# Kernel tuning notes

Measured on AMD Instinct MI355X. Metric: run time of the kernel, lower is better.

The kernel has to match this reference:

```python
import jax, jax.numpy as jnp
import numpy as np

COS_EPS = 1e-8  # torch F.cosine_similarity eps


def setup_inputs() -> dict:
    key = jax.random.key(0)
    k1, k2 = jax.random.split(key)
    x = jax.random.normal(k1, (8192, 512), dtype=jnp.float32)
    class_logits = jax.random.normal(k2, (8192, 100), dtype=jnp.float32)
    return {"x": x, "class_logits": class_logits}


def reference(x, class_logits):
    N, D = x.shape
    C = class_logits.shape[1]

    # class_logits.clone().detach()
    logits = jax.lax.stop_gradient(class_logits)
    pred = jax.nn.softmax(logits, axis=1)
    max_logit = pred.max(axis=1)          # [N]
    max_cls = pred.argmax(axis=1)         # [N] int

    # graph(): pairwise cosine similarity = normalize rows + gram matmul
    norms = jnp.linalg.norm(x, axis=1, keepdims=True)
    xn = x / jnp.maximum(norms, COS_EPS)
    mat = xn @ xn.T                       # [N, N]

    x_agg = mat @ x + x                   # [N, D]
    x_new = jax.lax.stop_gradient(x_agg)

    # update_prototype: per-class weighted scatter-add then mean over counts
    weighted = x_new * max_logit[:, None]                     # [N, D]
    sums = jax.ops.segment_sum(weighted, max_cls, num_segments=C)      # [C, D]
    counts = jax.ops.segment_sum(jnp.ones((N,), x.dtype), max_cls, num_segments=C)  # [C]
    prototypes = jnp.where(counts[:, None] > 0,
                           sums / jnp.maximum(counts, 1.0)[:, None],
                           jnp.zeros_like(sums))              # [C, D]

    # inter_class_matrix[i, j] = prototypes[j] - prototypes[i]
    inter_class_matrix = prototypes[None, :, :] - prototypes[:, None, :]  # [C, C, D]
    return prototypes, inter_class_matrix
```

## Files before the change

kernel.cpp:

```cpp
#include <hip/hip_runtime.h>
#include <math.h>

#define N_ROWS 8192
#define D_DIM  512
#define C_CLS  100

typedef unsigned short u16;
typedef unsigned int u32;
typedef __attribute__((ext_vector_type(8))) short short8;
typedef __attribute__((ext_vector_type(4))) float floatx4;

#define WS_G      0
#define WS_GP     262144
#define WS_INV    5505024
#define WS_SINV   5513216
#define WS_WV     5521408
#define WS_CLS    5529600
#define WS_CNT    5537792
#define WS_OFFS   5537920
#define WS_ORDER  5538048
#define WS_ZTH    5546240
#define WS_ZTL    7643392
#define WS_U      9740544
#define WS_V      9791744

__device__ __forceinline__ void split2(float v, u16& h, u16& l) {
    unsigned u = __float_as_uint(v);
    h = (u16)(u >> 16);
    float r = v - __uint_as_float(u & 0xFFFF0000u);
    l = (u16)(__float_as_uint(r) >> 16);
}

typedef const __attribute__((address_space(1))) u32* gp32;
typedef __attribute__((address_space(3))) u32* lp32;
__device__ __forceinline__ void cp16(const u16* g, u16* l) {
    __builtin_amdgcn_global_load_lds((gp32)g, (lp32)l, 16, 0, 0);
}

__global__ __launch_bounds__(256) void k_prep(const float* __restrict__ logits,
        const float* __restrict__ x, float* __restrict__ wv,
        int* __restrict__ cls, float* __restrict__ inv, float* __restrict__ sinv) {
    int wave = (blockIdx.x * blockDim.x + threadIdx.x) >> 6;
    int lane = threadIdx.x & 63;
    if (wave >= N_ROWS) return;
    const float* row = logits + (size_t)wave * C_CLS;
    float v1 = row[lane];
    bool has2 = (lane + 64) < C_CLS;
    float v2 = has2 ? row[lane + 64] : -INFINITY;
    float m; int idx;
    if (v2 > v1) { m = v2; idx = lane + 64; } else { m = v1; idx = lane; }
    #pragma unroll
    for (int off = 32; off >= 1; off >>= 1) {
        float om = __shfl_down(m, off);
        int   oi = __shfl_down(idx, off);
        if (om > m || (om == m && oi < idx)) { m = om; idx = oi; }
    }
    m = __shfl(m, 0);
    idx = __shfl(idx, 0);
    float s = expf(v1 - m) + (has2 ? expf(v2 - m) : 0.0f);
    #pragma unroll
    for (int off = 32; off >= 1; off >>= 1) s += __shfl_down(s, off);
    const float* xr = x + (size_t)wave * D_DIM;
    float ss = 0.f;
    #pragma unroll
    for (int j = 0; j < D_DIM; j += 64) {
        float v = xr[j + lane];
        ss += v * v;
    }
    #pragma unroll
    for (int off = 32; off >= 1; off >>= 1) ss += __shfl_down(ss, off);
    if (lane == 0) {
        wv[wave] = 1.0f / s;
        cls[wave] = idx;
        float iv = 1.0f / fmaxf(sqrtf(ss), 1e-8f);
        inv[wave] = iv;
        sinv[wave] = sqrtf(iv);
    }
}

#define LDT 65
__global__ __launch_bounds__(256) void k_mid(const float* __restrict__ x,
        const float* __restrict__ sinv, const int* __restrict__ cls,
        u16* __restrict__ zth, u16* __restrict__ ztl,
        int* __restrict__ cnt, int* __restrict__ offs, int* __restrict__ order) {
    __shared__ unsigned zt_p[64 * LDT];
    int bx = blockIdx.x;
    int t = threadIdx.x;
    if (bx == 1024) {
        __shared__ int hist[128], scan_s[128], cur[128];
        if (t < 128) hist[t] = 0;
        __syncthreads();
        for (int m2 = t; m2 < N_ROWS; m2 += 256) atomicAdd(&hist[cls[m2]], 1);
        __syncthreads();
        if (t < 128) scan_s[t] = hist[t];
        __syncthreads();
        #pragma unroll
        for (int d = 1; d < 128; d <<= 1) {
            int add = 0;
            if (t < 128 && t >= d) add = scan_s[t - d];
            __syncthreads();
            if (t < 128) scan_s[t] += add;
            __syncthreads();
        }
        if (t < 128) {
            int off0 = scan_s[t] - hist[t];
            cur[t] = off0;
            offs[t] = off0;
            cnt[t] = hist[t];
        }
        __syncthreads();
        for (int m2 = t; m2 < N_ROWS; m2 += 256) {
            int c2 = cls[m2];
            int p = atomicAdd(&cur[c2], 1);
            order[p] = m2;
        }
        return;
    }
    int r0 = (bx & 127) << 6, c0 = (bx >> 7) << 6;
    int r = t >> 2, cq = t & 3;
    const float* src = x + (size_t)(r0 + r) * D_DIM + c0 + cq * 16;
    float vv[16];
    {
        float4 a = *(const float4*)(src + 0);
        float4 b = *(const float4*)(src + 4);
        float4 c = *(const float4*)(src + 8);
        float4 d = *(const float4*)(src + 12);
        vv[0]=a.x; vv[1]=a.y; vv[2]=a.z; vv[3]=a.w;
        vv[4]=b.x; vv[5]=b.y; vv[6]=b.z; vv[7]=b.w;
        vv[8]=c.x; vv[9]=c.y; vv[10]=c.z; vv[11]=c.w;
        vv[12]=d.x; vv[13]=d.y; vv[14]=d.z; vv[15]=d.w;
    }
    float sv = sinv[r0 + r];
    #pragma unroll
    for (int j = 0; j < 16; ++j) {
        u16 h, l;
        split2(sv * vv[j], h, l);
        zt_p[(cq * 16 + j) * LDT + r] = ((unsigned)h << 16) | l;
    }
    __syncthreads();
    int c = t >> 2, rq = (t & 3) * 16;
    size_t tbase = (size_t)(c0 + c) * N_ROWS + r0 + rq;
    uint oh[8], ol[8];
    #pragma unroll
    for (int p = 0; p < 8; ++p) {
        unsigned d0 = zt_p[c * LDT + rq + 2*p];
        unsigned d1 = zt_p[c * LDT + rq + 2*p + 1];
        oh[p] = (d0 >> 16) | (d1 & 0xFFFF0000u);
        ol[p] = (d0 & 0xFFFFu) | (d1 << 16);
    }
    *(uint4*)&zth[tbase]     = make_uint4(oh[0], oh[1], oh[2], oh[3]);
    *(uint4*)&zth[tbase + 8] = make_uint4(oh[4], oh[5], oh[6], oh[7]);
    *(uint4*)&ztl[tbase]     = make_uint4(ol[0], ol[1], ol[2], ol[3]);
    *(uint4*)&ztl[tbase + 8] = make_uint4(ol[4], ol[5], ol[6], ol[7]);
}

__global__ __launch_bounds__(256) void k_big(const u16* __restrict__ zth,
        const u16* __restrict__ ztl, const float* __restrict__ x,
        const float* __restrict__ inv, const float* __restrict__ wv,
        const int* __restrict__ order, const int* __restrict__ offs,
        const int* __restrict__ cnt, float* __restrict__ Gp,
        float* __restrict__ u, float* __restrict__ v) {
    __shared__ __attribute__((aligned(16))) u16 Ah[128*32], Al[128*32];
    __shared__ __attribute__((aligned(16))) u16 Bh[128*32], Bl[128*32];
    __shared__ float us[4][64], vs[4][64];
    int bx = blockIdx.x;
    int t = threadIdx.x;
    if (bx >= 320) {
        int idx = bx - 320;
        int c = idx >> 3, jc = idx & 7;
        int g = t >> 6, lane = t & 63;
        int j = jc * 64 + lane;
        int n = cnt[c], o = offs[c];
        float ua = 0.f, va = 0.f;
        for (int p = g; p < n; p += 4) {
            int m = order[o + p];
            float wm = wv[m];
            float wi = wm * inv[m];
            float xv = x[(size_t)m * D_DIM + j];
            ua += wi * xv; va += wm * xv;
        }
        us[g][lane] = ua; vs[g][lane] = va;
        __syncthreads();
        if (g == 0) {
            u[(size_t)c * D_DIM + j] = us[0][lane] + us[1][lane] + us[2][lane] + us[3][lane];
            v[(size_t)c * D_DIM + j] = vs[0][lane] + vs[1][lane] + vs[2][lane] + vs[3][lane];
        }
        return;
    }
    int tile = bx % 10;
    int p = bx / 10;
    int ti = tile < 4 ? 0 : (tile < 7 ? 1 : (tile < 9 ? 2 : 3));
    int tj = tile - (ti == 0 ? 0 : (ti == 1 ? 3 : (ti == 2 ? 5 : 6)));
    int i0 = ti << 7, j0 = tj << 7;
    bool diag = (ti == tj);
    int kb = p << 8;
    int w = t >> 6, l = t & 63;
    int srow = t >> 2, scol = (t & 3) << 3;
    int lm = l & 15, lg = l >> 4;
    floatx4 acc[4][4];
    #pragma unroll
    for (int mi = 0; mi < 4; ++mi)
        #pragma unroll
        for (int ni = 0; ni < 4; ++ni) acc[mi][ni] = (floatx4){0.f,0.f,0.f,0.f};
    int d0 = srow * 32 + scol;
    int d1 = (64 + srow) * 32 + scol;
    const size_t ga0 = (size_t)(i0 + srow) * N_ROWS + kb + scol;
    const size_t ga1 = (size_t)(i0 + 64 + srow) * N_ROWS + kb + scol;
    const size_t gb0 = (size_t)(j0 + srow) * N_ROWS + kb + scol;
    const size_t gb1 = (size_t)(j0 + 64 + srow) * N_ROWS + kb + scol;
    const u16* Bhs = diag ? Ah : Bh;
    const u16* Bls = diag ? Al : Bl;
    for (int s = 0; s < 8; ++s) {
        int ks = s << 5;
        cp16(zth + ga0 + ks, Ah + d0);
        cp16(zth + ga1 + ks, Ah + d1);
        cp16(ztl + ga0 + ks, Al + d0);
        cp16(ztl + ga1 + ks, Al + d1);
        if (!diag) {
            cp16(zth + gb0 + ks, Bh + d0);
            cp16(zth + gb1 + ks, Bh + d1);
            cp16(ztl + gb0 + ks, Bl + d0);
            cp16(ztl + gb1 + ks, Bl + d1);
        }
        __syncthreads();
        short8 ah[4], al[4], bh[4], bl[4];
        #pragma unroll
        for (int mi = 0; mi < 4; ++mi) {
            int off = (((w & 1) << 6) + (mi << 4) + lm) * 32 + (lg << 3);
            ah[mi] = *(const short8*)&Ah[off];
            al[mi] = *(const short8*)&Al[off];
        }
        #pragma unroll
        for (int ni = 0; ni < 4; ++ni) {
            int off = (((w >> 1) << 6) + (ni << 4) + lm) * 32 + (lg << 3);
            bh[ni] = *(const short8*)&Bhs[off];
            bl[ni] = *(const short8*)&Bls[off];
        }
        #pragma unroll
        for (int mi = 0; mi < 4; ++mi)
            #pragma unroll
            for (int ni = 0; ni < 4; ++ni) {
                acc[mi][ni] = __builtin_amdgcn_mfma_f32_16x16x32_bf16(ah[mi], bh[ni], acc[mi][ni], 0, 0, 0);
                acc[mi][ni] = __builtin_amdgcn_mfma_f32_16x16x32_bf16(ah[mi], bl[ni], acc[mi][ni], 0, 0, 0);
                acc[mi][ni] = __builtin_amdgcn_mfma_f32_16x16x32_bf16(al[mi], bh[ni], acc[mi][ni], 0, 0, 0);
            }
        __syncthreads();
    }
    float* Gb = Gp + ((size_t)(p * 10 + tile) << 14);
    #pragma unroll
    for (int mi = 0; mi < 4; ++mi) {
        int row0 = ((w & 1) << 6) + (mi << 4) + (lg << 2);
        #pragma unroll
        for (int ni = 0; ni < 4; ++ni) {
            int col = ((w >> 1) << 6) + (ni << 4) + lm;
            #pragma unroll
            for (int r = 0; r < 4; ++r)
                Gb[(size_t)(row0 + r) * 128 + col] = acc[mi][ni][r];
        }
    }
}

__global__ void k_reduceG(const float* __restrict__ Gp, float* __restrict__ G) {
    int i = blockIdx.x * 256 + threadIdx.x;
    int r = i >> 9, c = i & 511;
    int tr = r >> 7, tc = c >> 7, rr = r & 127, cc = c & 127;
    if (tr > tc) { int tmp = tr; tr = tc; tc = tmp; tmp = rr; rr = cc; cc = tmp; }
    int tid = tr * 4 + tc - ((tr * (tr + 1)) >> 1);
    const float* src = Gp + ((size_t)tid << 14) + rr * 128 + cc;
    float s = 0.f;
    #pragma unroll
    for (int p = 0; p < 32; ++p) s += src[(size_t)p * 163840];
    G[i] = s;
}

__global__ __launch_bounds__(256) void k_pgemm(const float* __restrict__ u,
        const float* __restrict__ v, const int* __restrict__ cnt,
        const float* __restrict__ G, float* __restrict__ out) {
    __shared__ float us[D_DIM];
    int c = blockIdx.x >> 1;
    int j = ((blockIdx.x & 1) << 8) + threadIdx.x;
    us[threadIdx.x]       = u[(size_t)c * D_DIM + threadIdx.x];
    us[threadIdx.x + 256] = u[(size_t)c * D_DIM + threadIdx.x + 256];
    __syncthreads();
    float acc = v[(size_t)c * D_DIM + j];
    #pragma unroll 8
    for (int k = 0; k < D_DIM; ++k)
        acc += us[k] * G[(size_t)k * D_DIM + j];
    int n = cnt[c];
    float s = (n > 0) ? 1.0f / (float)n : 0.0f;
    out[(size_t)c * D_DIM + j] = acc * s;
}

__global__ void k_inter(const float* __restrict__ proto, float* __restrict__ out) {
    int pair = blockIdx.x;
    int i = pair / C_CLS;
    int j = pair - i * C_CLS;
    int d = threadIdx.x << 2;
    float4 pj = *(const float4*)&proto[j * D_DIM + d];
    float4 pi = *(const float4*)&proto[i * D_DIM + d];
    float4 r;
    r.x = pj.x - pi.x; r.y = pj.y - pi.y; r.z = pj.z - pi.z; r.w = pj.w - pi.w;
    *(float4*)&out[(size_t)pair * D_DIM + d] = r;
}

extern "C" void kernel_launch(void* const* d_in, const int* in_sizes, int n_in,
                              void* d_out, int out_size, void* d_ws, size_t ws_size,
                              hipStream_t stream) {
    const float* x      = (const float*)d_in[0];
    const float* logits = (const float*)d_in[1];
    float* out = (float*)d_out;
    float* ws  = (float*)d_ws;
    float* G     = ws + WS_G;
    float* Gp    = ws + WS_GP;
    float* inv   = ws + WS_INV;
    float* sinv  = ws + WS_SINV;
    float* wv    = ws + WS_WV;
    int*   cls   = (int*)(ws + WS_CLS);
    int*   cnt   = (int*)(ws + WS_CNT);
    int*   offs  = (int*)(ws + WS_OFFS);
    int*   order = (int*)(ws + WS_ORDER);
    u16* zth = (u16*)(ws + WS_ZTH);
    u16* ztl = (u16*)(ws + WS_ZTL);
    float* u_arr = ws + WS_U;
    float* v_arr = ws + WS_V;

    k_prep<<<N_ROWS / 4, 256, 0, stream>>>(logits, x, wv, cls, inv, sinv);
    k_mid<<<1025, 256, 0, stream>>>(x, sinv, cls, zth, ztl, cnt, offs, order);
    k_big<<<1120, 256, 0, stream>>>(zth, ztl, x, inv, wv, order, offs, cnt, Gp, u_arr, v_arr);
    k_reduceG<<<D_DIM * D_DIM / 256, 256, 0, stream>>>(Gp, G);
    k_pgemm<<<C_CLS * 2, 256, 0, stream>>>(u_arr, v_arr, cnt, G, out);
    k_inter<<<C_CLS * C_CLS, 128, 0, stream>>>(out, out + C_CLS * D_DIM);
}
```

Before: 178.8 us.

## Fuse prep kernels, replace split-K partial buffer with atomic accumulation

Folds row-norm computation, softmax stats and the hi/lo transpose split into one kernel, and moves the class histogram into its own single-block kernel. The Gram kernel now runs with a split-K depth of 512 instead of 256, halving the grid, and accumulates its tiles straight into G with float atomics, mirroring off-diagonal tiles, so the partial buffer and reduction kernel go away. The inter-class difference kernel handles 4 pairs per block with 8 floats per thread. This cuts launches and the partial-buffer traffic, at the cost of heavy atomic contention (16 partitions per element, doubled for off-diagonal tiles), nondeterministic summation order, and less parallelism in the GEMM.

```diff
diff --git a/kernel.cpp b/kernel.cpp
--- a/kernel.cpp
+++ b/kernel.cpp
@@ -11,18 +11,18 @@
 typedef __attribute__((ext_vector_type(4))) float floatx4;
 
 #define WS_G      0
-#define WS_GP     262144
-#define WS_INV    5505024
-#define WS_SINV   5513216
-#define WS_WV     5521408
-#define WS_CLS    5529600
-#define WS_CNT    5537792
-#define WS_OFFS   5537920
-#define WS_ORDER  5538048
-#define WS_ZTH    5546240
-#define WS_ZTL    7643392
-#define WS_U      9740544
-#define WS_V      9791744
+#define WS_INV    262144
+#define WS_WV     270336
+#define WS_CLS    278528
+#define WS_CNT    286720
+#define WS_OFFS   286848
+#define WS_ORDER  286976
+#define WS_U      295168
+#define WS_V      346368
+#define WS_ZTH    397568
+#define WS_ZTL    2494720
+
+#define LDT 65
 
 __device__ __forceinline__ void split2(float v, u16& h, u16& l) {
     unsigned u = __float_as_uint(v);
@@ -37,136 +37,151 @@
     __builtin_amdgcn_global_load_lds((gp32)g, (lp32)l, 16, 0, 0);
 }
 
-__global__ __launch_bounds__(256) void k_prep(const float* __restrict__ logits,
-        const float* __restrict__ x, float* __restrict__ wv,
-        int* __restrict__ cls, float* __restrict__ inv, float* __restrict__ sinv) {
-    int wave = (blockIdx.x * blockDim.x + threadIdx.x) >> 6;
-    int lane = threadIdx.x & 63;
-    if (wave >= N_ROWS) return;
-    const float* row = logits + (size_t)wave * C_CLS;
-    float v1 = row[lane];
-    bool has2 = (lane + 64) < C_CLS;
-    float v2 = has2 ? row[lane + 64] : -INFINITY;
-    float m; int idx;
-    if (v2 > v1) { m = v2; idx = lane + 64; } else { m = v1; idx = lane; }
+__global__ __launch_bounds__(256) void kA(const float* __restrict__ logits,
+        const float* __restrict__ x, float* __restrict__ wv, int* __restrict__ cls,
+        float* __restrict__ inv, u16* __restrict__ zth, u16* __restrict__ ztl,
+        float* __restrict__ G) {
+    __shared__ unsigned zt_p[64 * LDT];
+    __shared__ float ns[4][64];
+    __shared__ float sv_s[64];
+    int bx = blockIdx.x, t = threadIdx.x;
+    if (bx < 2048) {
+        int row = (bx << 2) + (t >> 6);
+        int lane = t & 63;
+        const float* lrow = logits + (size_t)row * C_CLS;
+        float v1 = lrow[lane];
+        bool has2 = (lane + 64) < C_CLS;
+        float v2 = has2 ? lrow[lane + 64] : -INFINITY;
+        float m; int idx;
+        if (v2 > v1) { m = v2; idx = lane + 64; } else { m = v1; idx = lane; }
+        #pragma unroll
+        for (int off = 32; off >= 1; off >>= 1) {
+            float om = __shfl_down(m, off);
+            int   oi = __shfl_down(idx, off);
+            if (om > m || (om == m && oi < idx)) { m = om; idx = oi; }
+        }
+        m = __shfl(m, 0);
+        idx = __shfl(idx, 0);
+        float s = expf(v1 - m) + (has2 ? expf(v2 - m) : 0.0f);
+        #pragma unroll
+        for (int off = 32; off >= 1; off >>= 1) s += __shfl_down(s, off);
+        if (lane == 0) {
+            wv[row] = 1.0f / s;
+            cls[row] = idx;
+        }
+        return;
+    }
+    if (bx >= 2176) {
+        int i = ((bx - 2176) * 256 + t) * 32;
+        float4 z = make_float4(0.f, 0.f, 0.f, 0.f);
+        #pragma unroll
+        for (int q = 0; q < 8; ++q) *(float4*)&G[i + q * 4] = z;
+        return;
+    }
+    int r0 = (bx - 2048) << 6;
+    {
+        int l = t & 63, q = t >> 6;
+        const float* src = x + (size_t)(r0 + l) * D_DIM + q * 128;
+        float ss = 0.f;
+        #pragma unroll
+        for (int i = 0; i < 32; ++i) {
+            float4 v = *(const float4*)(src + i * 4);
+            ss += v.x * v.x + v.y * v.y + v.z * v.z + v.w * v.w;
+        }
+        ns[q][l] = ss;
+    }
+    __syncthreads();
+    if (t < 64) {
+        float ss = ns[0][t] + ns[1][t] + ns[2][t] + ns[3][t];
+        float iv = 1.0f / fmaxf(sqrtf(ss), 1e-8f);
+        inv[r0 + t] = iv;
+        sv_s[t] = sqrtf(iv);
+    }
+    __syncthreads();
+    for (int ct = 0; ct < 8; ++ct) {
+        int c0 = ct * 64;
+        int r = t >> 2, cq = t & 3;
+        const float* src = x + (size_t)(r0 + r) * D_DIM + c0 + cq * 16;
+        float vv[16];
+        {
+            float4 a = *(const float4*)(src + 0);
+            float4 b = *(const float4*)(src + 4);
+            float4 c = *(const float4*)(src + 8);
+            float4 d = *(const float4*)(src + 12);
+            vv[0]=a.x; vv[1]=a.y; vv[2]=a.z; vv[3]=a.w;
+            vv[4]=b.x; vv[5]=b.y; vv[6]=b.z; vv[7]=b.w;
+            vv[8]=c.x; vv[9]=c.y; vv[10]=c.z; vv[11]=c.w;
+            vv[12]=d.x; vv[13]=d.y; vv[14]=d.z; vv[15]=d.w;
+        }
+        float sv = sv_s[r];
+        #pragma unroll
+        for (int j = 0; j < 16; ++j) {
+            u16 h, l;
+            split2(sv * vv[j], h, l);
+            zt_p[(cq * 16 + j) * LDT + r] = ((unsigned)h << 16) | l;
+        }
+        __syncthreads();
+        int c = t >> 2, rq = (t & 3) * 16;
+        size_t tbase = (size_t)(c0 + c) * N_ROWS + r0 + rq;
+        uint oh[8], ol[8];
+        #pragma unroll
+        for (int p = 0; p < 8; ++p) {
+            unsigned d0 = zt_p[c * LDT + rq + 2*p];
+            unsigned d1 = zt_p[c * LDT + rq + 2*p + 1];
+            oh[p] = (d0 >> 16) | (d1 & 0xFFFF0000u);
+            ol[p] = (d0 & 0xFFFFu) | (d1 << 16);
+        }
+        *(uint4*)&zth[tbase]     = make_uint4(oh[0], oh[1], oh[2], oh[3]);
+        *(uint4*)&zth[tbase + 8] = make_uint4(oh[4], oh[5], oh[6], oh[7]);
+        *(uint4*)&ztl[tbase]     = make_uint4(ol[0], ol[1], ol[2], ol[3]);
+        *(uint4*)&ztl[tbase + 8] = make_uint4(ol[4], ol[5], ol[6], ol[7]);
+        __syncthreads();
+    }
+}
+
+__global__ __launch_bounds__(256) void kB(const int* __restrict__ cls,
+        int* __restrict__ cnt, int* __restrict__ offs, int* __restrict__ order) {
+    __shared__ int hist[128], scan_s[128], cur[128];
+    int t = threadIdx.x;
+    if (t < 128) hist[t] = 0;
+    __syncthreads();
+    for (int m = t; m < N_ROWS; m += 256) atomicAdd(&hist[cls[m]], 1);
+    __syncthreads();
+    if (t < 128) scan_s[t] = hist[t];
+    __syncthreads();
     #pragma unroll
-    for (int off = 32; off >= 1; off >>= 1) {
-        float om = __shfl_down(m, off);
-        int   oi = __shfl_down(idx, off);
-        if (om > m || (om == m && oi < idx)) { m = om; idx = oi; }
-    }
-    m = __shfl(m, 0);
-    idx = __shfl(idx, 0);
-    float s = expf(v1 - m) + (has2 ? expf(v2 - m) : 0.0f);
-    #pragma unroll
-    for (int off = 32; off >= 1; off >>= 1) s += __shfl_down(s, off);
-    const float* xr = x + (size_t)wave * D_DIM;
-    float ss = 0.f;
-    #pragma unroll
-    for (int j = 0; j < D_DIM; j += 64) {
-        float v = xr[j + lane];
-        ss += v * v;
-    }
-    #pragma unroll
-    for (int off = 32; off >= 1; off >>= 1) ss += __shfl_down(ss, off);
-    if (lane == 0) {
-        wv[wave] = 1.0f / s;
-        cls[wave] = idx;
-        float iv = 1.0f / fmaxf(sqrtf(ss), 1e-8f);
-        inv[wave] = iv;
-        sinv[wave] = sqrtf(iv);
-    }
-}
-
-#define LDT 65
-__global__ __launch_bounds__(256) void k_mid(const float* __restrict__ x,
-        const float* __restrict__ sinv, const int* __restrict__ cls,
-        u16* __restrict__ zth, u16* __restrict__ ztl,
-        int* __restrict__ cnt, int* __restrict__ offs, int* __restrict__ order) {
-    __shared__ unsigned zt_p[64 * LDT];
-    int bx = blockIdx.x;
-    int t = threadIdx.x;
-    if (bx == 1024) {
-        __shared__ int hist[128], scan_s[128], cur[128];
-        if (t < 128) hist[t] = 0;
-        __syncthreads();
-        for (int m2 = t; m2 < N_ROWS; m2 += 256) atomicAdd(&hist[cls[m2]], 1);
-        __syncthreads();
-        if (t < 128) scan_s[t] = hist[t];
-        __syncthreads();
-        #pragma unroll
-        for (int d = 1; d < 128; d <<= 1) {
-            int add = 0;
-            if (t < 128 && t >= d) add = scan_s[t - d];
-            __syncthreads();
-            if (t < 128) scan_s[t] += add;
-            __syncthreads();
-        }
-        if (t < 128) {
-            int off0 = scan_s[t] - hist[t];
-            cur[t] = off0;
-            offs[t] = off0;
-            cnt[t] = hist[t];
-        }
-        __syncthreads();
-        for (int m2 = t; m2 < N_ROWS; m2 += 256) {
-            int c2 = cls[m2];
-            int p = atomicAdd(&cur[c2], 1);
-            order[p] = m2;
-        }
-        return;
-    }
-    int r0 = (bx & 127) << 6, c0 = (bx >> 7) << 6;
-    int r = t >> 2, cq = t & 3;
-    const float* src = x + (size_t)(r0 + r) * D_DIM + c0 + cq * 16;
-    float vv[16];
-    {
-        float4 a = *(const float4*)(src + 0);
-        float4 b = *(const float4*)(src + 4);
-        float4 c = *(const float4*)(src + 8);
-        float4 d = *(const float4*)(src + 12);
-        vv[0]=a.x; vv[1]=a.y; vv[2]=a.z; vv[3]=a.w;
-        vv[4]=b.x; vv[5]=b.y; vv[6]=b.z; vv[7]=b.w;
-        vv[8]=c.x; vv[9]=c.y; vv[10]=c.z; vv[11]=c.w;
-        vv[12]=d.x; vv[13]=d.y; vv[14]=d.z; vv[15]=d.w;
-    }
-    float sv = sinv[r0 + r];
-    #pragma unroll
-    for (int j = 0; j < 16; ++j) {
-        u16 h, l;
-        split2(sv * vv[j], h, l);
-        zt_p[(cq * 16 + j) * LDT + r] = ((unsigned)h << 16) | l;
-    }
-    __syncthreads();
-    int c = t >> 2, rq = (t & 3) * 16;
-    size_t tbase = (size_t)(c0 + c) * N_ROWS + r0 + rq;
-    uint oh[8], ol[8];
-    #pragma unroll
-    for (int p = 0; p < 8; ++p) {
-        unsigned d0 = zt_p[c * LDT + rq + 2*p];
-        unsigned d1 = zt_p[c * LDT + rq + 2*p + 1];
-        oh[p] = (d0 >> 16) | (d1 & 0xFFFF0000u);
-        ol[p] = (d0 & 0xFFFFu) | (d1 << 16);
-    }
-    *(uint4*)&zth[tbase]     = make_uint4(oh[0], oh[1], oh[2], oh[3]);
-    *(uint4*)&zth[tbase + 8] = make_uint4(oh[4], oh[5], oh[6], oh[7]);
-    *(uint4*)&ztl[tbase]     = make_uint4(ol[0], ol[1], ol[2], ol[3]);
-    *(uint4*)&ztl[tbase + 8] = make_uint4(ol[4], ol[5], ol[6], ol[7]);
-}
-
-__global__ __launch_bounds__(256) void k_big(const u16* __restrict__ zth,
+    for (int d = 1; d < 128; d <<= 1) {
+        int add = (t < 128 && t >= d) ? scan_s[t - d] : 0;
+        __syncthreads();
+        if (t < 128) scan_s[t] += add;
+        __syncthreads();
+    }
+    if (t < 128) {
+        int off0 = scan_s[t] - hist[t];
+        cur[t] = off0;
+        offs[t] = off0;
+        cnt[t] = hist[t];
+    }
+    __syncthreads();
+    for (int m = t; m < N_ROWS; m += 256) {
+        int p = atomicAdd(&cur[cls[m]], 1);
+        order[p] = m;
+    }
+}
+
+__global__ __launch_bounds__(256) void kC(const u16* __restrict__ zth,
         const u16* __restrict__ ztl, const float* __restrict__ x,
         const float* __restrict__ inv, const float* __restrict__ wv,
         const int* __restrict__ order, const int* __restrict__ offs,
-        const int* __restrict__ cnt, float* __restrict__ Gp,
-        float* __restrict__ u, float* __restrict__ v) {
-    __shared__ __attribute__((aligned(16))) u16 Ah[128*32], Al[128*32];
-    __shared__ __attribute__((aligned(16))) u16 Bh[128*32], Bl[128*32];
-    __shared__ float us[4][64], vs[4][64];
-    int bx = blockIdx.x;
-    int t = threadIdx.x;
-    if (bx >= 320) {
-        int idx = bx - 320;
+        const int* __restrict__ cnt, float* __restrict__ G,
+        float* __restrict__ u_arr, float* __restrict__ v_arr) {
+    __shared__ __attribute__((aligned(16))) union {
+        struct { u16 Ah[128*32], Al[128*32], Bh[128*32], Bl[128*32]; } g;
+        struct { float us[4][64], vs[4][64]; } uv;
+    } sm;
+    int bx = blockIdx.x, t = threadIdx.x;
+    if (bx >= 160) {
+        int idx = bx - 160;
         int c = idx >> 3, jc = idx & 7;
         int g = t >> 6, lane = t & 63;
         int j = jc * 64 + lane;
@@ -179,11 +194,11 @@
             float xv = x[(size_t)m * D_DIM + j];
             ua += wi * xv; va += wm * xv;
         }
-        us[g][lane] = ua; vs[g][lane] = va;
+        sm.uv.us[g][lane] = ua; sm.uv.vs[g][lane] = va;
         __syncthreads();
         if (g == 0) {
-            u[(size_t)c * D_DIM + j] = us[0][lane] + us[1][lane] + us[2][lane] + us[3][lane];
-            v[(size_t)c * D_DIM + j] = vs[0][lane] + vs[1][lane] + vs[2][lane] + vs[3][lane];
+            u_arr[(size_t)c * D_DIM + j] = sm.uv.us[0][lane] + sm.uv.us[1][lane] + sm.uv.us[2][lane] + sm.uv.us[3][lane];
+            v_arr[(size_t)c * D_DIM + j] = sm.uv.vs[0][lane] + sm.uv.vs[1][lane] + sm.uv.vs[2][lane] + sm.uv.vs[3][lane];
         }
         return;
     }
@@ -193,7 +208,7 @@
     int tj = tile - (ti == 0 ? 0 : (ti == 1 ? 3 : (ti == 2 ? 5 : 6)));
     int i0 = ti << 7, j0 = tj << 7;
     bool diag = (ti == tj);
-    int kb = p << 8;
+    int kb = p << 9;
     int w = t >> 6, l = t & 63;
     int srow = t >> 2, scol = (t & 3) << 3;
     int lm = l & 15, lg = l >> 4;
@@ -208,27 +223,27 @@
     const size_t ga1 = (size_t)(i0 + 64 + srow) * N_ROWS + kb + scol;
     const size_t gb0 = (size_t)(j0 + srow) * N_ROWS + kb + scol;
     const size_t gb1 = (size_t)(j0 + 64 + srow) * N_ROWS + kb + scol;
-    const u16* Bhs = diag ? Ah : Bh;
-    const u16* Bls = diag ? Al : Bl;
-    for (int s = 0; s < 8; ++s) {
+    const u16* Bhs = diag ? sm.g.Ah : sm.g.Bh;
+    const u16* Bls = diag ? sm.g.Al : sm.g.Bl;
+    for (int s = 0; s < 16; ++s) {
         int ks = s << 5;
-        cp16(zth + ga0 + ks, Ah + d0);
-        cp16(zth + ga1 + ks, Ah + d1);
-        cp16(ztl + ga0 + ks, Al + d0);
-        cp16(ztl + ga1 + ks, Al + d1);
+        cp16(zth + ga0 + ks, sm.g.Ah + d0);
+        cp16(zth + ga1 + ks, sm.g.Ah + d1);
+        cp16(ztl + ga0 + ks, sm.g.Al + d0);
+        cp16(ztl + ga1 + ks, sm.g.Al + d1);
         if (!diag) {
-            cp16(zth + gb0 + ks, Bh + d0);
-            cp16(zth + gb1 + ks, Bh + d1);
-            cp16(ztl + gb0 + ks, Bl + d0);
-            cp16(ztl + gb1 + ks, Bl + d1);
+            cp16(zth + gb0 + ks, sm.g.Bh + d0);
+            cp16(zth + gb1 + ks, sm.g.Bh + d1);
+            cp16(ztl + gb0 + ks, sm.g.Bl + d0);
+            cp16(ztl + gb1 + ks, sm.g.Bl + d1);
         }
         __syncthreads();
         short8 ah[4], al[4], bh[4], bl[4];
         #pragma unroll
         for (int mi = 0; mi < 4; ++mi) {
             int off = (((w & 1) << 6) + (mi << 4) + lm) * 32 + (lg << 3);
-            ah[mi] = *(const short8*)&Ah[off];
-            al[mi] = *(const short8*)&Al[off];
+            ah[mi] = *(const short8*)&sm.g.Ah[off];
+            al[mi] = *(const short8*)&sm.g.Al[off];
         }
         #pragma unroll
         for (int ni = 0; ni < 4; ++ni) {
@@ -246,61 +261,56 @@
             }
         __syncthreads();
     }
-    float* Gb = Gp + ((size_t)(p * 10 + tile) << 14);
     #pragma unroll
     for (int mi = 0; mi < 4; ++mi) {
-        int row0 = ((w & 1) << 6) + (mi << 4) + (lg << 2);
+        int row0 = i0 + ((w & 1) << 6) + (mi << 4) + (lg << 2);
         #pragma unroll
         for (int ni = 0; ni < 4; ++ni) {
-            int col = ((w >> 1) << 6) + (ni << 4) + lm;
+            int col = j0 + ((w >> 1) << 6) + (ni << 4) + lm;
             #pragma unroll
-            for (int r = 0; r < 4; ++r)
-                Gb[(size_t)(row0 + r) * 128 + col] = acc[mi][ni][r];
-        }
-    }
-}
-
-__global__ void k_reduceG(const float* __restrict__ Gp, float* __restrict__ G) {
-    int i = blockIdx.x * 256 + threadIdx.x;
-    int r = i >> 9, c = i & 511;
-    int tr = r >> 7, tc = c >> 7, rr = r & 127, cc = c & 127;
-    if (tr > tc) { int tmp = tr; tr = tc; tc = tmp; tmp = rr; rr = cc; cc = tmp; }
-    int tid = tr * 4 + tc - ((tr * (tr + 1)) >> 1);
-    const float* src = Gp + ((size_t)tid << 14) + rr * 128 + cc;
-    float s = 0.f;
-    #pragma unroll
-    for (int p = 0; p < 32; ++p) s += src[(size_t)p * 163840];
-    G[i] = s;
-}
-
-__global__ __launch_bounds__(256) void k_pgemm(const float* __restrict__ u,
-        const float* __restrict__ v, const int* __restrict__ cnt,
+            for (int r = 0; r < 4; ++r) {
+                float val = acc[mi][ni][r];
+                atomicAdd(&G[(size_t)(row0 + r) * D_DIM + col], val);
+                if (!diag)
+                    atomicAdd(&G[(size_t)col * D_DIM + (row0 + r)], val);
+            }
+        }
+    }
+}
+
+__global__ __launch_bounds__(256) void kD(const float* __restrict__ u_arr,
+        const float* __restrict__ v_arr, const int* __restrict__ cnt,
         const float* __restrict__ G, float* __restrict__ out) {
-    __shared__ float us[D_DIM];
+    __shared__ float ug[D_DIM];
     int c = blockIdx.x >> 1;
     int j = ((blockIdx.x & 1) << 8) + threadIdx.x;
-    us[threadIdx.x]       = u[(size_t)c * D_DIM + threadIdx.x];
-    us[threadIdx.x + 256] = u[(size_t)c * D_DIM + threadIdx.x + 256];
-    __syncthreads();
-    float acc = v[(size_t)c * D_DIM + j];
+    ug[threadIdx.x]       = u_arr[(size_t)c * D_DIM + threadIdx.x];
+    ug[threadIdx.x + 256] = u_arr[(size_t)c * D_DIM + threadIdx.x + 256];
+    __syncthreads();
+    float acc = v_arr[(size_t)c * D_DIM + j];
     #pragma unroll 8
     for (int k = 0; k < D_DIM; ++k)
-        acc += us[k] * G[(size_t)k * D_DIM + j];
+        acc += ug[k] * G[(size_t)k * D_DIM + j];
     int n = cnt[c];
     float s = (n > 0) ? 1.0f / (float)n : 0.0f;
     out[(size_t)c * D_DIM + j] = acc * s;
 }
 
-__global__ void k_inter(const float* __restrict__ proto, float* __restrict__ out) {
-    int pair = blockIdx.x;
+__global__ __launch_bounds__(256) void kE(const float* __restrict__ proto,
+                                          float* __restrict__ inter) {
+    int pair = blockIdx.x * 4 + (threadIdx.x >> 6);
     int i = pair / C_CLS;
     int j = pair - i * C_CLS;
-    int d = threadIdx.x << 2;
-    float4 pj = *(const float4*)&proto[j * D_DIM + d];
-    float4 pi = *(const float4*)&proto[i * D_DIM + d];
-    float4 r;
-    r.x = pj.x - pi.x; r.y = pj.y - pi.y; r.z = pj.z - pi.z; r.w = pj.w - pi.w;
-    *(float4*)&out[(size_t)pair * D_DIM + d] = r;
+    int d = (threadIdx.x & 63) << 3;
+    float4 pj0 = *(const float4*)&proto[j * D_DIM + d];
+    float4 pj1 = *(const float4*)&proto[j * D_DIM + d + 4];
+    float4 pi0 = *(const float4*)&proto[i * D_DIM + d];
+    float4 pi1 = *(const float4*)&proto[i * D_DIM + d + 4];
+    float4 r0, r1;
+    r0.x = pj0.x - pi0.x; r0.y = pj0.y - pi0.y; r0.z = pj0.z - pi0.z; r0.w = pj0.w - pi0.w;
+    r1.x = pj1.x - pi1.x; r1.y = pj1.y - pi1.y; r1.z = pj1.z - pi1.z; r1.w = pj1.w - pi1.w;
+    *(float4*)&inter[(size_t)pair * D_DIM + d]     = r0;
+    *(float4*)&inter[(size_t)pair * D_DIM + d + 4] = r1;
 }
 
 extern "C" void kernel_launch(void* const* d_in, const int* in_sizes, int n_in,
@@ -311,23 +321,20 @@
     float* out = (float*)d_out;
     float* ws  = (float*)d_ws;
     float* G     = ws + WS_G;
-    float* Gp    = ws + WS_GP;
     float* inv   = ws + WS_INV;
-    float* sinv  = ws + WS_SINV;
     float* wv    = ws + WS_WV;
     int*   cls   = (int*)(ws + WS_CLS);
     int*   cnt   = (int*)(ws + WS_CNT);
     int*   offs  = (int*)(ws + WS_OFFS);
     int*   order = (int*)(ws + WS_ORDER);
+    float* u_arr = ws + WS_U;
+    float* v_arr = ws + WS_V;
     u16* zth = (u16*)(ws + WS_ZTH);
     u16* ztl = (u16*)(ws + WS_ZTL);
-    float* u_arr = ws + WS_U;
-    float* v_arr = ws + WS_V;
-
-    k_prep<<<N_ROWS / 4, 256, 0, stream>>>(logits, x, wv, cls, inv, sinv);
-    k_mid<<<1025, 256, 0, stream>>>(x, sinv, cls, zth, ztl, cnt, offs, order);
-    k_big<<<1120, 256, 0, stream>>>(zth, ztl, x, inv, wv, order, offs, cnt, Gp, u_arr, v_arr);
-    k_reduceG<<<D_DIM * D_DIM / 256, 256, 0, stream>>>(Gp, G);
-    k_pgemm<<<C_CLS * 2, 256, 0, stream>>>(u_arr, v_arr, cnt, G, out);
-    k_inter<<<C_CLS * C_CLS, 128, 0, stream>>>(out, out + C_CLS * D_DIM);
-}
+
+    kA<<<2208, 256, 0, stream>>>(logits, x, wv, cls, inv, zth, ztl, G);
+    kB<<<1, 256, 0, stream>>>(cls, cnt, offs, order);
+    kC<<<960, 256, 0, stream>>>(zth, ztl, x, inv, wv, order, offs, cnt, G, u_arr, v_arr);
+    kD<<<C_CLS * 2, 256, 0, stream>>>(u_arr, v_arr, cnt, G, out);
+    kE<<<C_CLS * C_CLS / 4, 256, 0, stream>>>(out, out + C_CLS * D_DIM);
+}
```

Result: slower. 185.6 us (+3.8%).
